# Performance work log

Hardware: AMD Instinct MI355X
Metric: run time of the kernel (lower is better)

## Reference

```python
import jax, jax.numpy as jnp
import numpy as np

N = 50000      # nodes
E = 1600000    # edges (avg degree 32)
D_IN = 32
D_EF = 16
D_H = 64
D_MSG = 32
D_UP = 32


def setup_inputs() -> dict:
    key = jax.random.key(0)
    ks = jax.random.split(key, 10)
    s = 0.05
    return {
        "x": jax.random.normal(ks[0], (N, D_IN), dtype=jnp.float32),
        "degrees": jax.random.uniform(ks[1], (N, 1), dtype=jnp.float32),
        "edge_features": jax.random.normal(ks[2], (E, D_EF), dtype=jnp.float32),
        "W1m": jax.random.normal(ks[3], (2 * D_IN + D_EF, D_H), dtype=jnp.float32) * s,
        "b1m": jnp.zeros((D_H,), dtype=jnp.float32),
        "W2m": jax.random.normal(ks[4], (D_H, D_MSG), dtype=jnp.float32) * s,
        "b2m": jnp.zeros((D_MSG,), dtype=jnp.float32),
        "W1u": jax.random.normal(ks[5], (D_IN + D_MSG, D_H), dtype=jnp.float32) * s,
        "b1u": jnp.zeros((D_H,), dtype=jnp.float32),
        "W2u": jax.random.normal(ks[6], (D_H, D_UP), dtype=jnp.float32) * s,
        "b2u": jnp.zeros((D_UP,), dtype=jnp.float32),
        "edge_index": jax.random.randint(ks[7], (2, E), 0, N, dtype=jnp.int64),
    }


def mlp2(h, W1, b1, W2, b2):
    return jax.nn.relu(h @ W1 + b1) @ W2 + b2


def reference(x, degrees, edge_features, W1m, b1m, W2m, b2m, W1u, b1u, W2u, b2u, edge_index):
    # flow = 'source_to_target': select=1 -> i = targets = edge_index[1],
    # j = sources = edge_index[0]; sparse.sum over dim 0 aggregates per target.
    src = edge_index[0]
    dst = edge_index[1]
    x_i = x[dst]                                  # [E, D_IN] target features
    x_j = x[src]                                  # [E, D_IN] source features
    msg_in = jnp.concatenate([x_i, x_j, edge_features], axis=-1)  # [E, 2*D_IN+D_EF]
    msgs = mlp2(msg_in, W1m, b1m, W2m, b2m)       # [E, D_MSG]
    agg = jax.ops.segment_sum(msgs, dst, num_segments=x.shape[0])  # [N, D_MSG]
    upd_in = jnp.concatenate([x, agg], axis=-1)   # [N, D_IN+D_MSG]
    return mlp2(upd_in, W1u, b1u, W2u, b2u)       # [N, D_UP]
```

## Files before the change

kernel.cpp:

```cpp
#include <hip/hip_runtime.h>
#include <hip/hip_bf16.h>

#define D_IN  32
#define D_EF  16
#define D_H   64
#define D_MSG 32
#define D_UP  32

typedef __fp16 v2h __attribute__((ext_vector_type(2)));

__device__ __forceinline__ unsigned bf16pair(float a, float b) {
    unsigned ua = __float_as_uint(a);
    ua = (ua + 0x7fffu + ((ua >> 16) & 1u)) >> 16;
    unsigned ub = __float_as_uint(b);
    ub = (ub + 0x7fffu + ((ub >> 16) & 1u)) >> 16;
    return ua | (ub << 16);
}
__device__ __forceinline__ float bf_lo(unsigned u) { return __uint_as_float(u << 16); }
__device__ __forceinline__ float bf_hi(unsigned u) { return __uint_as_float(u & 0xffff0000u); }

__global__ __launch_bounds__(256) void prep_kernel(
    const float* __restrict__ x,
    const float* __restrict__ W1m,
    const float* __restrict__ b1m,
    const int*   __restrict__ ei,
    float* __restrict__ P1,
    unsigned short* __restrict__ P2b,
    int* __restrict__ deg,
    int* __restrict__ rank,
    v2h* __restrict__ W1Ep,
    int n_nodes, int n_edges, int NBn, int NBe)
{
    int b = blockIdx.x;

    if (b < NBn) {
        int i = b * 256 + threadIdx.x;
        if (i >= n_nodes) return;

        float xi[D_IN];
        const float4* xp = (const float4*)(x + (size_t)i * D_IN);
#pragma unroll
        for (int k4 = 0; k4 < D_IN / 4; ++k4) {
            float4 v = xp[k4];
            xi[4 * k4 + 0] = v.x; xi[4 * k4 + 1] = v.y;
            xi[4 * k4 + 2] = v.z; xi[4 * k4 + 3] = v.w;
        }
        {
            float acc[D_H];
#pragma unroll
            for (int j = 0; j < D_H; ++j) acc[j] = b1m[j];
            for (int k = 0; k < D_IN; ++k) {
                float xv = xi[k];
                const float* wr = W1m + (size_t)k * D_H;
#pragma unroll
                for (int j = 0; j < D_H; ++j) acc[j] += xv * wr[j];
            }
            float4* o = (float4*)(P1 + (size_t)i * D_H);
#pragma unroll
            for (int j4 = 0; j4 < D_H / 4; ++j4)
                o[j4] = make_float4(acc[4 * j4], acc[4 * j4 + 1],
                                    acc[4 * j4 + 2], acc[4 * j4 + 3]);
        }
        {
            float acc[D_H];
#pragma unroll
            for (int j = 0; j < D_H; ++j) acc[j] = 0.0f;
            for (int k = 0; k < D_IN; ++k) {
                float xv = xi[k];
                const float* wr = W1m + (size_t)(k + D_IN) * D_H;
#pragma unroll
                for (int j = 0; j < D_H; ++j) acc[j] += xv * wr[j];
            }
            uint4* o = (uint4*)(P2b + (size_t)i * D_H);
#pragma unroll
            for (int j8 = 0; j8 < D_H / 8; ++j8) {
                uint4 q;
                q.x = bf16pair(acc[8 * j8 + 0], acc[8 * j8 + 1]);
                q.y = bf16pair(acc[8 * j8 + 2], acc[8 * j8 + 3]);
                q.z = bf16pair(acc[8 * j8 + 4], acc[8 * j8 + 5]);
                q.w = bf16pair(acc[8 * j8 + 6], acc[8 * j8 + 7]);
                o[j8] = q;
            }
        }
    } else if (b < NBn + NBe) {
        int e = (b - NBn) * 256 + threadIdx.x;
        if (e < n_edges)
            rank[e] = atomicAdd(&deg[ei[n_edges + e]], 1);
    } else {
        int t = threadIdx.x;
        const float* W1E = W1m + (size_t)(2 * D_IN) * D_H;
        for (int idx = t; idx < 8 * D_H; idx += 256) {
            int kp = idx >> 6, c = idx & 63;
            W1Ep[idx] = __builtin_amdgcn_cvt_pkrtz(W1E[(2 * kp) * D_H + c],
                                                   W1E[(2 * kp + 1) * D_H + c]);
        }
    }
}

__global__ __launch_bounds__(256) void scan_partials_kernel(
    const int* __restrict__ deg, int* __restrict__ bsum, int n_nodes)
{
    int idx = blockIdx.x * 256 + threadIdx.x;
    int v = (idx < n_nodes) ? deg[idx] : 0;
#pragma unroll
    for (int o = 1; o < 64; o <<= 1) v += __shfl_xor(v, o, 64);
    __shared__ int ws[4];
    int lane = threadIdx.x & 63, w = threadIdx.x >> 6;
    if (lane == 0) ws[w] = v;
    __syncthreads();
    if (threadIdx.x == 0) bsum[blockIdx.x] = ws[0] + ws[1] + ws[2] + ws[3];
}

__global__ __launch_bounds__(256) void scan_blockoffs_kernel(
    const int* __restrict__ bsum, int* __restrict__ boffs, int nb)
{
    __shared__ int sdata[256];
    int t = threadIdx.x;
    sdata[t] = (t < nb) ? bsum[t] : 0;
    __syncthreads();
    for (int off = 1; off < 256; off <<= 1) {
        int u = (t >= off) ? sdata[t - off] : 0;
        __syncthreads();
        sdata[t] += u;
        __syncthreads();
    }
    if (t < nb) boffs[t] = (t > 0) ? sdata[t - 1] : 0;
}

__global__ __launch_bounds__(256) void scan_final_kernel(
    const int* __restrict__ deg, const int* __restrict__ boffs,
    int* __restrict__ offs, int n_nodes)
{
    __shared__ int sdata[256];
    int t = threadIdx.x;
    int idx = blockIdx.x * 256 + t;
    sdata[t] = (idx < n_nodes) ? deg[idx] : 0;
    __syncthreads();
    for (int off = 1; off < 256; off <<= 1) {
        int u = (t >= off) ? sdata[t - off] : 0;
        __syncthreads();
        sdata[t] += u;
        __syncthreads();
    }
    int excl = boffs[blockIdx.x] + ((t > 0) ? sdata[t - 1] : 0);
    if (idx < n_nodes) offs[idx] = excl;
}

__global__ __launch_bounds__(256) void scatter_kernel(
    const int* __restrict__ ei,
    const int* __restrict__ rank,
    const int* __restrict__ offs,
    int2* __restrict__ edges_sorted,
    int n_edges)
{
    int e = blockIdx.x * blockDim.x + threadIdx.x;
    if (e < n_edges) {
        int s = ei[e];
        int d = ei[n_edges + e];
        int pos = offs[d] + rank[e];
        edges_sorted[pos] = make_int2(e, s);
    }
}

__global__ __launch_bounds__(256, 6) void gather_kernel(
    const float* __restrict__ ef,
    const v2h*  __restrict__ W1Ep,
    const float* __restrict__ P1,
    const unsigned short* __restrict__ P2b,
    const int*  __restrict__ deg,
    const int*  __restrict__ offs,
    const int2* __restrict__ edges_sorted,
    float* __restrict__ hagg,
    int n_nodes)
{
    const int lane = threadIdx.x & 63;
    const int cg   = __builtin_amdgcn_readfirstlane((int)(threadIdx.x >> 6));
    const int g    = lane >> 4;
    const int t    = lane & 15;
    const int n    = blockIdx.x * 4 + g;
    if (n >= n_nodes) return;

    const int start = offs[n];
    const int end   = start + deg[n];

    float p1q[16];
    {
        const float4* pp = (const float4*)(P1 + (size_t)n * D_H + cg * 16);
#pragma unroll
        for (int q = 0; q < 4; ++q) {
            float4 v = pp[q];
            p1q[4 * q + 0] = v.x; p1q[4 * q + 1] = v.y;
            p1q[4 * q + 2] = v.z; p1q[4 * q + 3] = v.w;
        }
    }

    const v2h* wbase = W1Ep + 16 * cg;

    float hacc[16];
#pragma unroll
    for (int c = 0; c < 16; ++c) hacc[c] = 0.0f;

    for (int i = start + t; i < end; i += 16) {
        int2 es = edges_sorted[i];
        const float4* efp = (const float4*)(ef + (size_t)es.x * D_EF);
        float4 f0 = efp[0], f1 = efp[1], f2 = efp[2], f3 = efp[3];
        const uint4* p2u = (const uint4*)(P2b + (size_t)es.y * D_H + cg * 16);
        uint4 b0 = p2u[0], b1 = p2u[1];

        v2h efh[D_EF / 2];
        efh[0] = __builtin_amdgcn_cvt_pkrtz(f0.x, f0.y);
        efh[1] = __builtin_amdgcn_cvt_pkrtz(f0.z, f0.w);
        efh[2] = __builtin_amdgcn_cvt_pkrtz(f1.x, f1.y);
        efh[3] = __builtin_amdgcn_cvt_pkrtz(f1.z, f1.w);
        efh[4] = __builtin_amdgcn_cvt_pkrtz(f2.x, f2.y);
        efh[5] = __builtin_amdgcn_cvt_pkrtz(f2.z, f2.w);
        efh[6] = __builtin_amdgcn_cvt_pkrtz(f3.x, f3.y);
        efh[7] = __builtin_amdgcn_cvt_pkrtz(f3.z, f3.w);

#pragma unroll
        for (int jj = 0; jj < 2; ++jj) {
            uint4 b = jj ? b1 : b0;
            float h[8];
            h[0] = p1q[8 * jj + 0] + bf_lo(b.x);
            h[1] = p1q[8 * jj + 1] + bf_hi(b.x);
            h[2] = p1q[8 * jj + 2] + bf_lo(b.y);
            h[3] = p1q[8 * jj + 3] + bf_hi(b.y);
            h[4] = p1q[8 * jj + 4] + bf_lo(b.z);
            h[5] = p1q[8 * jj + 5] + bf_hi(b.z);
            h[6] = p1q[8 * jj + 6] + bf_lo(b.w);
            h[7] = p1q[8 * jj + 7] + bf_hi(b.w);

#pragma unroll
            for (int kp = 0; kp < D_EF / 2; ++kp) {
                const v2h* wr = wbase + kp * D_H + 8 * jj;
#pragma unroll
                for (int c8 = 0; c8 < 8; ++c8)
                    h[c8] = __builtin_amdgcn_fdot2(efh[kp], wr[c8], h[c8], false);
            }

#pragma unroll
            for (int c8 = 0; c8 < 8; ++c8) {
                float r = h[c8] > 0.0f ? h[c8] : 0.0f;
                hacc[8 * jj + c8] += r;
            }
        }
    }

    float r1[8];
    {
        const bool up = (t & 8) != 0;
#pragma unroll
        for (int c = 0; c < 8; ++c) {
            float lo = hacc[c]     + __shfl_xor(hacc[c],     8, 16);
            float hi = hacc[c + 8] + __shfl_xor(hacc[c + 8], 8, 16);
            r1[c] = up ? hi : lo;
        }
    }
    float r2[4];
    {
        const bool up = (t & 4) != 0;
#pragma unroll
        for (int c = 0; c < 4; ++c) {
            float lo = r1[c]     + __shfl_xor(r1[c],     4, 16);
            float hi = r1[c + 4] + __shfl_xor(r1[c + 4], 4, 16);
            r2[c] = up ? hi : lo;
        }
    }
    float r3[2];
    {
        const bool up = (t & 2) != 0;
#pragma unroll
        for (int c = 0; c < 2; ++c) {
            float lo = r2[c]     + __shfl_xor(r2[c],     2, 16);
            float hi = r2[c + 2] + __shfl_xor(r2[c + 2], 2, 16);
            r3[c] = up ? hi : lo;
        }
    }
    float r4;
    {
        const bool up = (t & 1) != 0;
        float lo = r3[0] + __shfl_xor(r3[0], 1, 16);
        float hi = r3[1] + __shfl_xor(r3[1], 1, 16);
        r4 = up ? hi : lo;
    }

    hagg[(size_t)n * D_H + cg * 16 + t] = r4;
}

__global__ __launch_bounds__(256) void node_upd_kernel(
    const float* __restrict__ x,
    const float* __restrict__ hagg,
    const int*   __restrict__ deg,
    const float* __restrict__ b2m,
    const float* __restrict__ W2m,
    const float* __restrict__ W1u,
    const float* __restrict__ b1u,
    const float* __restrict__ W2u,
    const float* __restrict__ b2u,
    float* __restrict__ out,
    int n_nodes)
{
    int i = blockIdx.x * blockDim.x + threadIdx.x;
    if (i >= n_nodes) return;

    float in[D_IN + D_MSG];
    const float4* xp = (const float4*)(x + (size_t)i * D_IN);
#pragma unroll
    for (int k4 = 0; k4 < D_IN / 4; ++k4) {
        float4 v = xp[k4];
        in[4 * k4 + 0] = v.x; in[4 * k4 + 1] = v.y;
        in[4 * k4 + 2] = v.z; in[4 * k4 + 3] = v.w;
    }

    float dc = (float)deg[i];
#pragma unroll
    for (int m = 0; m < D_MSG; ++m) in[D_IN + m] = dc * b2m[m];

    const float4* hp = (const float4*)(hagg + (size_t)i * D_H);
    for (int j4 = 0; j4 < D_H / 4; ++j4) {
        float4 v = hp[j4];
        const float* w0 = W2m + (size_t)(4 * j4 + 0) * D_MSG;
        const float* w1 = W2m + (size_t)(4 * j4 + 1) * D_MSG;
        const float* w2 = W2m + (size_t)(4 * j4 + 2) * D_MSG;
        const float* w3 = W2m + (size_t)(4 * j4 + 3) * D_MSG;
#pragma unroll
        for (int m = 0; m < D_MSG; ++m)
            in[D_IN + m] += v.x * w0[m] + v.y * w1[m] + v.z * w2[m] + v.w * w3[m];
    }

    float h[D_H];
#pragma unroll
    for (int j = 0; j < D_H; ++j) h[j] = b1u[j];
    for (int k = 0; k < D_IN + D_MSG; ++k) {
        float v = in[k];
        const float* wr = W1u + (size_t)k * D_H;
#pragma unroll
        for (int j = 0; j < D_H; ++j) h[j] += v * wr[j];
    }

    float o[D_UP];
#pragma unroll
    for (int m = 0; m < D_UP; ++m) o[m] = b2u[m];
    for (int j = 0; j < D_H; ++j) {
        float r = h[j] > 0.0f ? h[j] : 0.0f;
        const float* wr = W2u + (size_t)j * D_UP;
#pragma unroll
        for (int m = 0; m < D_UP; ++m) o[m] += r * wr[m];
    }

    float4* op = (float4*)(out + (size_t)i * D_UP);
#pragma unroll
    for (int m4 = 0; m4 < D_UP / 4; ++m4)
        op[m4] = make_float4(o[4 * m4], o[4 * m4 + 1], o[4 * m4 + 2], o[4 * m4 + 3]);
}

extern "C" void kernel_launch(void* const* d_in, const int* in_sizes, int n_in,
                              void* d_out, int out_size, void* d_ws, size_t ws_size,
                              hipStream_t stream) {
    const float* x    = (const float*)d_in[0];
    const float* ef   = (const float*)d_in[2];
    const float* W1m  = (const float*)d_in[3];
    const float* b1m  = (const float*)d_in[4];
    const float* W2m  = (const float*)d_in[5];
    const float* b2m  = (const float*)d_in[6];
    const float* W1u  = (const float*)d_in[7];
    const float* b1u  = (const float*)d_in[8];
    const float* W2u  = (const float*)d_in[9];
    const float* b2u  = (const float*)d_in[10];
    const int*   ei   = (const int*)d_in[11];

    const int n_nodes = in_sizes[0] / D_IN;
    const int n_edges = in_sizes[11] / 2;

    float* out = (float*)d_out;

    const int NBn = (n_nodes + 255) / 256;
    const int NBe = (n_edges + 255) / 256;

    float*          P1  = (float*)d_ws;
    unsigned short* P2b = (unsigned short*)(P1 + (size_t)n_nodes * D_H);
    int2* edges_sorted  = (int2*)(P2b + (size_t)n_nodes * D_H);
    int* deg    = (int*)(edges_sorted + n_edges);
    int* offs   = deg    + n_nodes;
    int* bsum   = offs   + n_nodes;
    int* boffs  = bsum   + NBn;
    v2h* W1Ep   = (v2h*)(boffs + NBn);
    int*   rank = (int*)(W1Ep + 8 * D_H);
    float* hagg = (float*)rank;

    hipMemsetAsync(deg, 0, (size_t)n_nodes * sizeof(int), stream);

    prep_kernel<<<NBn + NBe + 1, 256, 0, stream>>>(
        x, W1m, b1m, ei, P1, P2b, deg, rank, W1Ep,
        n_nodes, n_edges, NBn, NBe);

    scan_partials_kernel<<<NBn, 256, 0, stream>>>(deg, bsum, n_nodes);
    scan_blockoffs_kernel<<<1, 256, 0, stream>>>(bsum, boffs, NBn);
    scan_final_kernel<<<NBn, 256, 0, stream>>>(deg, boffs, offs, n_nodes);

    scatter_kernel<<<NBe, 256, 0, stream>>>(ei, rank, offs, edges_sorted, n_edges);

    {
        int grid = (n_nodes + 3) / 4;
        gather_kernel<<<grid, 256, 0, stream>>>(ef, W1Ep, P1, P2b,
                                                deg, offs, edges_sorted, hagg,
                                                n_nodes);
    }
    node_upd_kernel<<<NBn, 256, 0, stream>>>(x, hagg, deg, b2m, W2m,
                                             W1u, b1u, W2u, b2u, out, n_nodes);
}
```

Baseline: 450.0 us.

## Fuse node update into gather, pre-convert edge features to fp16, merge scan kernels

Fuses the node-update MLP into the gather kernel through shared memory, so the per-node hidden aggregate no longer makes a round trip through global memory and one launch disappears. Edge features are converted to packed fp16 in the prep kernel when workspace allows, halving the bytes read by each random gather in the hot loop, at the cost of an extra coalesced streaming pass over all edge features. The block-offset scan is folded into the final scan kernel, removing another launch. The gather kernel also drops its occupancy launch-bounds hint and adds a block barrier.

```diff
diff --git a/kernel.cpp b/kernel.cpp
--- a/kernel.cpp
+++ b/kernel.cpp
@@ -18,17 +18,22 @@
 }
 __device__ __forceinline__ float bf_lo(unsigned u) { return __uint_as_float(u << 16); }
 __device__ __forceinline__ float bf_hi(unsigned u) { return __uint_as_float(u & 0xffff0000u); }
+__device__ __forceinline__ v2h u2h(unsigned u) {
+    union { unsigned u; v2h h; } c; c.u = u; return c.h;
+}
 
 __global__ __launch_bounds__(256) void prep_kernel(
     const float* __restrict__ x,
     const float* __restrict__ W1m,
     const float* __restrict__ b1m,
+    const float* __restrict__ ef,
     const int*   __restrict__ ei,
     float* __restrict__ P1,
     unsigned short* __restrict__ P2b,
     int* __restrict__ deg,
     int* __restrict__ rank,
     v2h* __restrict__ W1Ep,
+    v2h* __restrict__ efh,
     int n_nodes, int n_edges, int NBn, int NBe)
 {
     int b = blockIdx.x;
@@ -86,7 +91,7 @@
         int e = (b - NBn) * 256 + threadIdx.x;
         if (e < n_edges)
             rank[e] = atomicAdd(&deg[ei[n_edges + e]], 1);
-    } else {
+    } else if (b == NBn + NBe) {
         int t = threadIdx.x;
         const float* W1E = W1m + (size_t)(2 * D_IN) * D_H;
         for (int idx = t; idx < 8 * D_H; idx += 256) {
@@ -94,10 +99,21 @@
             W1Ep[idx] = __builtin_amdgcn_cvt_pkrtz(W1E[(2 * kp) * D_H + c],
                                                    W1E[(2 * kp + 1) * D_H + c]);
         }
-    }
-}
-
-__global__ __launch_bounds__(256) void scan_partials_kernel(
+    } else {
+        int cb  = b - (NBn + NBe + 1);
+        int row = cb * 64 + (threadIdx.x >> 2);
+        int q   = threadIdx.x & 3;
+        if (row < n_edges) {
+            const float4* fp = (const float4*)(ef + (size_t)row * D_EF + q * 4);
+            float4 f = fp[0];
+            v2h* o = efh + (size_t)row * 8 + q * 2;
+            o[0] = __builtin_amdgcn_cvt_pkrtz(f.x, f.y);
+            o[1] = __builtin_amdgcn_cvt_pkrtz(f.z, f.w);
+        }
+    }
+}
+
+__global__ __launch_bounds__(256) void scan_reduce_kernel(
     const int* __restrict__ deg, int* __restrict__ bsum, int n_nodes)
 {
     int idx = blockIdx.x * 256 + threadIdx.x;
@@ -111,28 +127,24 @@
     if (threadIdx.x == 0) bsum[blockIdx.x] = ws[0] + ws[1] + ws[2] + ws[3];
 }
 
-__global__ __launch_bounds__(256) void scan_blockoffs_kernel(
-    const int* __restrict__ bsum, int* __restrict__ boffs, int nb)
+__global__ __launch_bounds__(256) void scan_final_kernel(
+    const int* __restrict__ deg, const int* __restrict__ bsum,
+    int* __restrict__ offs, int n_nodes, int nb)
 {
+    __shared__ int sb[256];
     __shared__ int sdata[256];
     int t = threadIdx.x;
-    sdata[t] = (t < nb) ? bsum[t] : 0;
+
+    sb[t] = (t < nb) ? bsum[t] : 0;
     __syncthreads();
     for (int off = 1; off < 256; off <<= 1) {
-        int u = (t >= off) ? sdata[t - off] : 0;
+        int u = (t >= off) ? sb[t - off] : 0;
         __syncthreads();
-        sdata[t] += u;
+        sb[t] += u;
         __syncthreads();
     }
-    if (t < nb) boffs[t] = (t > 0) ? sdata[t - 1] : 0;
-}
-
-__global__ __launch_bounds__(256) void scan_final_kernel(
-    const int* __restrict__ deg, const int* __restrict__ boffs,
-    int* __restrict__ offs, int n_nodes)
-{
-    __shared__ int sdata[256];
-    int t = threadIdx.x;
+    int base = (blockIdx.x > 0) ? sb[blockIdx.x - 1] : 0;
+
     int idx = blockIdx.x * 256 + t;
     sdata[t] = (idx < n_nodes) ? deg[idx] : 0;
     __syncthreads();
@@ -142,8 +154,7 @@
         sdata[t] += u;
         __syncthreads();
     }
-    int excl = boffs[blockIdx.x] + ((t > 0) ? sdata[t - 1] : 0);
-    if (idx < n_nodes) offs[idx] = excl;
+    if (idx < n_nodes) offs[idx] = base + ((t > 0) ? sdata[t - 1] : 0);
 }
 
 __global__ __launch_bounds__(256) void scatter_kernel(
@@ -162,135 +173,17 @@
     }
 }
 
-__global__ __launch_bounds__(256, 6) void gather_kernel(
+template<int USE_EFH>
+__global__ __launch_bounds__(256) void gather_kernel(
     const float* __restrict__ ef,
+    const v2h*  __restrict__ efh,
     const v2h*  __restrict__ W1Ep,
     const float* __restrict__ P1,
     const unsigned short* __restrict__ P2b,
     const int*  __restrict__ deg,
     const int*  __restrict__ offs,
     const int2* __restrict__ edges_sorted,
-    float* __restrict__ hagg,
-    int n_nodes)
-{
-    const int lane = threadIdx.x & 63;
-    const int cg   = __builtin_amdgcn_readfirstlane((int)(threadIdx.x >> 6));
-    const int g    = lane >> 4;
-    const int t    = lane & 15;
-    const int n    = blockIdx.x * 4 + g;
-    if (n >= n_nodes) return;
-
-    const int start = offs[n];
-    const int end   = start + deg[n];
-
-    float p1q[16];
-    {
-        const float4* pp = (const float4*)(P1 + (size_t)n * D_H + cg * 16);
-#pragma unroll
-        for (int q = 0; q < 4; ++q) {
-            float4 v = pp[q];
-            p1q[4 * q + 0] = v.x; p1q[4 * q + 1] = v.y;
-            p1q[4 * q + 2] = v.z; p1q[4 * q + 3] = v.w;
-        }
-    }
-
-    const v2h* wbase = W1Ep + 16 * cg;
-
-    float hacc[16];
-#pragma unroll
-    for (int c = 0; c < 16; ++c) hacc[c] = 0.0f;
-
-    for (int i = start + t; i < end; i += 16) {
-        int2 es = edges_sorted[i];
-        const float4* efp = (const float4*)(ef + (size_t)es.x * D_EF);
-        float4 f0 = efp[0], f1 = efp[1], f2 = efp[2], f3 = efp[3];
-        const uint4* p2u = (const uint4*)(P2b + (size_t)es.y * D_H + cg * 16);
-        uint4 b0 = p2u[0], b1 = p2u[1];
-
-        v2h efh[D_EF / 2];
-        efh[0] = __builtin_amdgcn_cvt_pkrtz(f0.x, f0.y);
-        efh[1] = __builtin_amdgcn_cvt_pkrtz(f0.z, f0.w);
-        efh[2] = __builtin_amdgcn_cvt_pkrtz(f1.x, f1.y);
-        efh[3] = __builtin_amdgcn_cvt_pkrtz(f1.z, f1.w);
-        efh[4] = __builtin_amdgcn_cvt_pkrtz(f2.x, f2.y);
-        efh[5] = __builtin_amdgcn_cvt_pkrtz(f2.z, f2.w);
-        efh[6] = __builtin_amdgcn_cvt_pkrtz(f3.x, f3.y);
-        efh[7] = __builtin_amdgcn_cvt_pkrtz(f3.z, f3.w);
-
-#pragma unroll
-        for (int jj = 0; jj < 2; ++jj) {
-            uint4 b = jj ? b1 : b0;
-            float h[8];
-            h[0] = p1q[8 * jj + 0] + bf_lo(b.x);
-            h[1] = p1q[8 * jj + 1] + bf_hi(b.x);
-            h[2] = p1q[8 * jj + 2] + bf_lo(b.y);
-            h[3] = p1q[8 * jj + 3] + bf_hi(b.y);
-            h[4] = p1q[8 * jj + 4] + bf_lo(b.z);
-            h[5] = p1q[8 * jj + 5] + bf_hi(b.z);
-            h[6] = p1q[8 * jj + 6] + bf_lo(b.w);
-            h[7] = p1q[8 * jj + 7] + bf_hi(b.w);
-
-#pragma unroll
-            for (int kp = 0; kp < D_EF / 2; ++kp) {
-                const v2h* wr = wbase + kp * D_H + 8 * jj;
-#pragma unroll
-                for (int c8 = 0; c8 < 8; ++c8)
-                    h[c8] = __builtin_amdgcn_fdot2(efh[kp], wr[c8], h[c8], false);
-            }
-
-#pragma unroll
-            for (int c8 = 0; c8 < 8; ++c8) {
-                float r = h[c8] > 0.0f ? h[c8] : 0.0f;
-                hacc[8 * jj + c8] += r;
-            }
-        }
-    }
-
-    float r1[8];
-    {
-        const bool up = (t & 8) != 0;
-#pragma unroll
-        for (int c = 0; c < 8; ++c) {
-            float lo = hacc[c]     + __shfl_xor(hacc[c],     8, 16);
-            float hi = hacc[c + 8] + __shfl_xor(hacc[c + 8], 8, 16);
-            r1[c] = up ? hi : lo;
-        }
-    }
-    float r2[4];
-    {
-        const bool up = (t & 4) != 0;
-#pragma unroll
-        for (int c = 0; c < 4; ++c) {
-            float lo = r1[c]     + __shfl_xor(r1[c],     4, 16);
-            float hi = r1[c + 4] + __shfl_xor(r1[c + 4], 4, 16);
-            r2[c] = up ? hi : lo;
-        }
-    }
-    float r3[2];
-    {
-        const bool up = (t & 2) != 0;
-#pragma unroll
-        for (int c = 0; c < 2; ++c) {
-            float lo = r2[c]     + __shfl_xor(r2[c],     2, 16);
-            float hi = r2[c + 2] + __shfl_xor(r2[c + 2], 2, 16);
-            r3[c] = up ? hi : lo;
-        }
-    }
-    float r4;
-    {
-        const bool up = (t & 1) != 0;
-        float lo = r3[0] + __shfl_xor(r3[0], 1, 16);
-        float hi = r3[1] + __shfl_xor(r3[1], 1, 16);
-        r4 = up ? hi : lo;
-    }
-
-    hagg[(size_t)n * D_H + cg * 16 + t] = r4;
-}
-
-__global__ __launch_bounds__(256) void node_upd_kernel(
     const float* __restrict__ x,
-    const float* __restrict__ hagg,
-    const int*   __restrict__ deg,
     const float* __restrict__ b2m,
     const float* __restrict__ W2m,
     const float* __restrict__ W1u,
@@ -300,58 +193,160 @@
     float* __restrict__ out,
     int n_nodes)
 {
-    int i = blockIdx.x * blockDim.x + threadIdx.x;
-    if (i >= n_nodes) return;
-
-    float in[D_IN + D_MSG];
-    const float4* xp = (const float4*)(x + (size_t)i * D_IN);
-#pragma unroll
-    for (int k4 = 0; k4 < D_IN / 4; ++k4) {
-        float4 v = xp[k4];
-        in[4 * k4 + 0] = v.x; in[4 * k4 + 1] = v.y;
-        in[4 * k4 + 2] = v.z; in[4 * k4 + 3] = v.w;
-    }
-
-    float dc = (float)deg[i];
-#pragma unroll
-    for (int m = 0; m < D_MSG; ++m) in[D_IN + m] = dc * b2m[m];
-
-    const float4* hp = (const float4*)(hagg + (size_t)i * D_H);
-    for (int j4 = 0; j4 < D_H / 4; ++j4) {
-        float4 v = hp[j4];
-        const float* w0 = W2m + (size_t)(4 * j4 + 0) * D_MSG;
-        const float* w1 = W2m + (size_t)(4 * j4 + 1) * D_MSG;
-        const float* w2 = W2m + (size_t)(4 * j4 + 2) * D_MSG;
-        const float* w3 = W2m + (size_t)(4 * j4 + 3) * D_MSG;
-#pragma unroll
-        for (int m = 0; m < D_MSG; ++m)
-            in[D_IN + m] += v.x * w0[m] + v.y * w1[m] + v.z * w2[m] + v.w * w3[m];
-    }
-
-    float h[D_H];
-#pragma unroll
-    for (int j = 0; j < D_H; ++j) h[j] = b1u[j];
-    for (int k = 0; k < D_IN + D_MSG; ++k) {
-        float v = in[k];
-        const float* wr = W1u + (size_t)k * D_H;
-#pragma unroll
-        for (int j = 0; j < D_H; ++j) h[j] += v * wr[j];
-    }
-
-    float o[D_UP];
-#pragma unroll
-    for (int m = 0; m < D_UP; ++m) o[m] = b2u[m];
-    for (int j = 0; j < D_H; ++j) {
-        float r = h[j] > 0.0f ? h[j] : 0.0f;
-        const float* wr = W2u + (size_t)j * D_UP;
-#pragma unroll
-        for (int m = 0; m < D_UP; ++m) o[m] += r * wr[m];
-    }
-
-    float4* op = (float4*)(out + (size_t)i * D_UP);
-#pragma unroll
-    for (int m4 = 0; m4 < D_UP / 4; ++m4)
-        op[m4] = make_float4(o[4 * m4], o[4 * m4 + 1], o[4 * m4 + 2], o[4 * m4 + 3]);
+    __shared__ float hs[4][64];
+    __shared__ float in2[4][64];
+    __shared__ float rh[4][64];
+
+    const int tid  = threadIdx.x;
+    const int lane = tid & 63;
+    const int cq   = __builtin_amdgcn_readfirstlane(tid >> 6);
+    const int g    = lane >> 4;
+    const int t    = lane & 15;
+    const int n    = blockIdx.x * 4 + g;
+    const bool valid = n < n_nodes;
+
+    int start = 0, end = 0;
+    if (valid) { start = offs[n]; end = start + deg[n]; }
+
+    float p1q[16];
+#pragma unroll
+    for (int q = 0; q < 16; ++q) p1q[q] = 0.0f;
+    if (valid) {
+        const float4* pp = (const float4*)(P1 + (size_t)n * D_H + cq * 16);
+#pragma unroll
+        for (int q = 0; q < 4; ++q) {
+            float4 v = pp[q];
+            p1q[4 * q + 0] = v.x; p1q[4 * q + 1] = v.y;
+            p1q[4 * q + 2] = v.z; p1q[4 * q + 3] = v.w;
+        }
+    }
+
+    const v2h* wbase = W1Ep + 16 * cq;
+
+    float hacc[16];
+#pragma unroll
+    for (int c = 0; c < 16; ++c) hacc[c] = 0.0f;
+
+    for (int i = start + t; i < end; i += 16) {
+        int2 es = edges_sorted[i];
+
+        v2h efr[8];
+        if (USE_EFH) {
+            const uint4* ep = (const uint4*)(efh + (size_t)(unsigned)es.x * 8);
+            uint4 u0 = ep[0], u1 = ep[1];
+            efr[0] = u2h(u0.x); efr[1] = u2h(u0.y);
+            efr[2] = u2h(u0.z); efr[3] = u2h(u0.w);
+            efr[4] = u2h(u1.x); efr[5] = u2h(u1.y);
+            efr[6] = u2h(u1.z); efr[7] = u2h(u1.w);
+        } else {
+            const float4* efp = (const float4*)(ef + (size_t)(unsigned)es.x * D_EF);
+            float4 f0 = efp[0], f1 = efp[1], f2 = efp[2], f3 = efp[3];
+            efr[0] = __builtin_amdgcn_cvt_pkrtz(f0.x, f0.y);
+            efr[1] = __builtin_amdgcn_cvt_pkrtz(f0.z, f0.w);
+            efr[2] = __builtin_amdgcn_cvt_pkrtz(f1.x, f1.y);
+            efr[3] = __builtin_amdgcn_cvt_pkrtz(f1.z, f1.w);
+            efr[4] = __builtin_amdgcn_cvt_pkrtz(f2.x, f2.y);
+            efr[5] = __builtin_amdgcn_cvt_pkrtz(f2.z, f2.w);
+            efr[6] = __builtin_amdgcn_cvt_pkrtz(f3.x, f3.y);
+            efr[7] = __builtin_amdgcn_cvt_pkrtz(f3.z, f3.w);
+        }
+
+        const uint4* p2u = (const uint4*)(P2b + (size_t)(unsigned)es.y * D_H + cq * 16);
+        uint4 b0 = p2u[0], b1 = p2u[1];
+
+#pragma unroll
+        for (int jj = 0; jj < 2; ++jj) {
+            uint4 bb = jj ? b1 : b0;
+            float h[8];
+            h[0] = p1q[8 * jj + 0] + bf_lo(bb.x);
+            h[1] = p1q[8 * jj + 1] + bf_hi(bb.x);
+            h[2] = p1q[8 * jj + 2] + bf_lo(bb.y);
+            h[3] = p1q[8 * jj + 3] + bf_hi(bb.y);
+            h[4] = p1q[8 * jj + 4] + bf_lo(bb.z);
+            h[5] = p1q[8 * jj + 5] + bf_hi(bb.z);
+            h[6] = p1q[8 * jj + 6] + bf_lo(bb.w);
+            h[7] = p1q[8 * jj + 7] + bf_hi(bb.w);
+#pragma unroll
+            for (int kp = 0; kp < D_EF / 2; ++kp) {
+                const v2h* wr = wbase + kp * D_H + 8 * jj;
+#pragma unroll
+                for (int c8 = 0; c8 < 8; ++c8)
+                    h[c8] = __builtin_amdgcn_fdot2(efr[kp], wr[c8], h[c8], false);
+            }
+#pragma unroll
+            for (int c8 = 0; c8 < 8; ++c8) {
+                float r = h[c8] > 0.0f ? h[c8] : 0.0f;
+                hacc[8 * jj + c8] += r;
+            }
+        }
+    }
+
+    float r1[8];
+    {
+        const bool up = (t & 8) != 0;
+#pragma unroll
+        for (int c = 0; c < 8; ++c) {
+            float lo = hacc[c]     + __shfl_xor(hacc[c],     8, 16);
+            float hi = hacc[c + 8] + __shfl_xor(hacc[c + 8], 8, 16);
+            r1[c] = up ? hi : lo;
+        }
+    }
+    float r2[4];
+    {
+        const bool up = (t & 4) != 0;
+#pragma unroll
+        for (int c = 0; c < 4; ++c) {
+            float lo = r1[c]     + __shfl_xor(r1[c],     4, 16);
+            float hi = r1[c + 4] + __shfl_xor(r1[c + 4], 4, 16);
+            r2[c] = up ? hi : lo;
+        }
+    }
+    float r3[2];
+    {
+        const bool up = (t & 2) != 0;
+#pragma unroll
+        for (int c = 0; c < 2; ++c) {
+            float lo = r2[c]     + __shfl_xor(r2[c],     2, 16);
+            float hi = r2[c + 2] + __shfl_xor(r2[c + 2], 2, 16);
+            r3[c] = up ? hi : lo;
+        }
+    }
+    float r4;
+    {
+        const bool up = (t & 1) != 0;
+        float lo = r3[0] + __shfl_xor(r3[0], 1, 16);
+        float hi = r3[1] + __shfl_xor(r3[1], 1, 16);
+        r4 = up ? hi : lo;
+    }
+
+    hs[g][cq * 16 + t] = r4;
+    __syncthreads();
+
+    const int nn = blockIdx.x * 4 + cq;
+    if (nn < n_nodes) {
+        if (lane < D_MSG) {
+            float a = (float)deg[nn] * b2m[lane];
+#pragma unroll 8
+            for (int k = 0; k < D_H; ++k)
+                a += hs[cq][k] * W2m[(size_t)k * D_MSG + lane];
+            in2[cq][D_IN + lane] = a;
+        } else {
+            in2[cq][lane - D_MSG] = x[(size_t)nn * D_IN + (lane - D_MSG)];
+        }
+        float hval = b1u[lane];
+#pragma unroll 8
+        for (int k = 0; k < D_IN + D_MSG; ++k)
+            hval += in2[cq][k] * W1u[(size_t)k * D_H + lane];
+        rh[cq][lane] = hval > 0.0f ? hval : 0.0f;
+
+        const int m = lane & 31;
+        float o = b2u[m];
+#pragma unroll 8
+        for (int j = 0; j < D_H; ++j)
+            o += rh[cq][j] * W2u[(size_t)j * D_UP + m];
+        if (lane < D_UP)
+            out[(size_t)nn * D_UP + m] = o;
+    }
 }
 
 extern "C" void kernel_launch(void* const* d_in, const int* in_sizes, int n_in,
@@ -376,6 +371,7 @@
 
     const int NBn = (n_nodes + 255) / 256;
     const int NBe = (n_edges + 255) / 256;
+    const int NBc = (n_edges + 63) / 64;
 
     float*          P1  = (float*)d_ws;
     unsigned short* P2b = (unsigned short*)(P1 + (size_t)n_nodes * D_H);
@@ -383,29 +379,36 @@
     int* deg    = (int*)(edges_sorted + n_edges);
     int* offs   = deg    + n_nodes;
     int* bsum   = offs   + n_nodes;
-    int* boffs  = bsum   + NBn;
-    v2h* W1Ep   = (v2h*)(boffs + NBn);
-    int*   rank = (int*)(W1Ep + 8 * D_H);
-    float* hagg = (float*)rank;
+    v2h* W1Ep   = (v2h*)(bsum + 256);
+    int* rank   = (int*)(W1Ep + 8 * D_H);
+    size_t efh_off = (((char*)(rank + n_edges) - (char*)d_ws) + 15) & ~(size_t)15;
+    v2h* efh    = (v2h*)((char*)d_ws + efh_off);
+    size_t need = efh_off + (size_t)n_edges * 8 * sizeof(v2h);
+    const bool use_efh = ws_size >= need;
 
     hipMemsetAsync(deg, 0, (size_t)n_nodes * sizeof(int), stream);
 
-    prep_kernel<<<NBn + NBe + 1, 256, 0, stream>>>(
-        x, W1m, b1m, ei, P1, P2b, deg, rank, W1Ep,
-        n_nodes, n_edges, NBn, NBe);
-
-    scan_partials_kernel<<<NBn, 256, 0, stream>>>(deg, bsum, n_nodes);
-    scan_blockoffs_kernel<<<1, 256, 0, stream>>>(bsum, boffs, NBn);
-    scan_final_kernel<<<NBn, 256, 0, stream>>>(deg, boffs, offs, n_nodes);
+    {
+        int grid = NBn + NBe + 1 + (use_efh ? NBc : 0);
+        prep_kernel<<<grid, 256, 0, stream>>>(
+            x, W1m, b1m, ef, ei, P1, P2b, deg, rank, W1Ep, efh,
+            n_nodes, n_edges, NBn, NBe);
+    }
+
+    scan_reduce_kernel<<<NBn, 256, 0, stream>>>(deg, bsum, n_nodes);
+    scan_final_kernel<<<NBn, 256, 0, stream>>>(deg, bsum, offs, n_nodes, NBn);
 
     scatter_kernel<<<NBe, 256, 0, stream>>>(ei, rank, offs, edges_sorted, n_edges);
 
     {
         int grid = (n_nodes + 3) / 4;
-        gather_kernel<<<grid, 256, 0, stream>>>(ef, W1Ep, P1, P2b,
-                                                deg, offs, edges_sorted, hagg,
-                                                n_nodes);
-    }
-    node_upd_kernel<<<NBn, 256, 0, stream>>>(x, hagg, deg, b2m, W2m,
-                                             W1u, b1u, W2u, b2u, out, n_nodes);
-}
+        if (use_efh)
+            gather_kernel<1><<<grid, 256, 0, stream>>>(
+                ef, efh, W1Ep, P1, P2b, deg, offs, edges_sorted,
+                x, b2m, W2m, W1u, b1u, W2u, b2u, out, n_nodes);
+        else
+            gather_kernel<0><<<grid, 256, 0, stream>>>(
+                ef, efh, W1Ep, P1, P2b, deg, offs, edges_sorted,
+                x, b2m, W2m, W1u, b1u, W2u, b2u, out, n_nodes);
+    }
+}
```

After: 582.6 us. 29.5% more time.
